# Kernel optimization log

Measured on AMD Instinct MI355X. Metric: run time of the kernel, lower is better.

## Reference

```python
import jax, jax.numpy as jnp
import numpy as np
import math

DIM = 256
N = 4096
E = 1024
NEG = -1.0e9


def setup_inputs() -> dict:
    key = jax.random.key(0)
    ks = jax.random.split(key, 10)
    x = jax.random.normal(ks[0], (N, DIM), dtype=jnp.float32)
    # sparse incidence / adjacency (module only uses >0 as mask)
    H = (jax.random.uniform(ks[1], (N, E)) < 0.05).astype(jnp.float32)
    adj = (jax.random.uniform(ks[2], (N, N)) < 0.01).astype(jnp.float32)
    s = 1.0 / math.sqrt(DIM)
    W_he = jax.random.normal(ks[3], (DIM, DIM), dtype=jnp.float32) * s  # HyperedgeAttention.W
    u = jax.random.normal(ks[4], (DIM,), dtype=jnp.float32)            # HyperedgeAttention.u
    W_e = jax.random.normal(ks[5], (DIM, DIM), dtype=jnp.float32) * s  # NodeAttention.W_e
    W_n = jax.random.normal(ks[6], (DIM, DIM), dtype=jnp.float32) * s  # NodeAttention.W_n
    W_g = jax.random.normal(ks[7], (DIM, DIM), dtype=jnp.float32) * s  # GraphAttention.W
    a_g = jax.random.normal(ks[8], (2 * DIM,), dtype=jnp.float32) * s  # GraphAttention.attn weight
    return {"x": x, "H": H, "adj": adj, "W_he": W_he, "u": u,
            "W_e": W_e, "W_n": W_n, "W_g": W_g, "a_g": a_g}


def reference(x, H, adj, W_he, u, W_e, W_n, W_g, a_g):
    n, dim = x.shape
    inv_sqrt_d = 1.0 / math.sqrt(dim)
    maskH = H > 0                       # [N,E] bool
    mask_Hf = maskH.astype(x.dtype)

    # ---- HyperedgeAttention ----
    h_he = x @ W_he                     # [N,dim]
    sc = (h_he @ u) * inv_sqrt_d        # [N]
    scE = jnp.where(maskH, sc[:, None], NEG)      # [N,E]
    A = jax.nn.softmax(scE, axis=0) * mask_Hf     # column softmax over nodes
    e_repr = A.T @ h_he                 # [E,dim]

    # ---- NodeAttention (only B is used) ----
    hn = x @ W_n                        # [N,dim]
    he = e_repr @ W_e                   # [E,dim]
    Bsc = jnp.where(maskH, (hn @ he.T) * inv_sqrt_d, NEG)
    B = jax.nn.softmax(Bsc, axis=1) * mask_Hf     # [N,E]

    # ---- GraphAttention (concat score split: e_ij = lrelu(h_i.a1 + h_j.a2)) ----
    h_g = x @ W_g                       # [N,dim]
    s1 = h_g @ a_g[:dim]                # [N]
    s2 = h_g @ a_g[dim:]                # [N]
    e = jax.nn.leaky_relu(s1[:, None] + s2[None, :], 0.2)   # [N,N]
    maskA = (adj > 0).astype(x.dtype)
    sl = jnp.eye(n, dtype=x.dtype)
    e = e * (maskA + sl) - 1e9 * jnp.clip(1.0 - maskA - sl, 0.0, None)
    G = jax.nn.softmax(e, axis=1)       # [N,N]

    # ---- Mixing ----
    he_sz = jnp.clip(mask_Hf.sum(0), 1.0, None)   # [E]
    M = (G @ mask_Hf) / he_sz[None, :]            # [N,E]
    A_hat = jax.nn.softmax(A.T + M.T, axis=1) * mask_Hf.T   # [E,N]
    e_mix = A_hat @ (x @ W_he)                    # [E,dim]
    B_hat = jax.nn.softmax(B + M, axis=1) * mask_Hf          # [N,E]
    z_h = jax.nn.elu(B_hat @ (e_mix @ W_e))       # [N,dim]
    G_hat = jax.nn.softmax(G + B @ B.T + A @ A.T, axis=1)    # [N,N]
    z_g = jax.nn.elu(G_hat @ (x @ W_g))           # [N,dim]
    return z_h, z_g
```

## Files before the change

### kernel.cpp

```cpp
#include <hip/hip_runtime.h>
#include <math.h>
#include <stdint.h>

#define Nn 4096
#define Ee 1024
#define Dd 256

typedef __attribute__((ext_vector_type(8))) __bf16 bf16x8;
typedef __attribute__((ext_vector_type(4))) float f32x4;
typedef __attribute__((ext_vector_type(8))) unsigned short u16x8;

__device__ __forceinline__ unsigned short f2bf(float f) {
  unsigned int u = __float_as_uint(f);
  unsigned int r = (u + 0x7fffu + ((u >> 16) & 1u)) >> 16;
  return (unsigned short)r;
}
__device__ __forceinline__ float bf2f(unsigned short u) {
  return __uint_as_float(((unsigned int)u) << 16);
}

__device__ __forceinline__ void gload_lds16(const void* g, void* l) {
  __builtin_amdgcn_global_load_lds(
      (__attribute__((address_space(1))) void*)const_cast<void*>(g),
      (__attribute__((address_space(3))) void*)l, 16, 0, 0);
}

__device__ __forceinline__ float block_reduce_sum(float v) {
  __shared__ float sh[4];
  #pragma unroll
  for (int o = 32; o > 0; o >>= 1) v += __shfl_down(v, o);
  int lane = threadIdx.x & 63, w = threadIdx.x >> 6;
  if (lane == 0) sh[w] = v;
  __syncthreads();
  float s = sh[0] + sh[1] + sh[2] + sh[3];
  __syncthreads();
  return s;
}

__global__ __launch_bounds__(256) void gemm_bt_bf16(
    const unsigned short* __restrict__ Ab, const unsigned short* __restrict__ Bb,
    float* __restrict__ Cp, unsigned short* __restrict__ Cb,
    int M, int N, int K, int lda, int ldb, float alpha)
{
  __shared__ unsigned short As[2][128 * 32];
  __shared__ unsigned short Bs[2][128 * 32];
  const int tid = threadIdx.x;
  const int m0 = blockIdx.x * 128, n0 = blockIdx.y * 128;
  const int wave = tid >> 6, lane = tid & 63;
  const int wr = (wave >> 1) * 64, wc = (wave & 1) * 64;
  const int l16 = lane & 15, lq = lane >> 4;
  f32x4 acc[4][4] = {};
  const int NT = K >> 5;

  auto stage = [&](int buf, int kt) {
    const int k0 = kt * 32;
    #pragma unroll
    for (int i = 0; i < 2; ++i) {
      int t2 = tid + i * 256;
      int r = t2 >> 2, c = (t2 & 3) * 8;
      gload_lds16(Ab + (size_t)(m0 + r) * lda + k0 + c, &As[buf][t2 * 8]);
    }
    #pragma unroll
    for (int i = 0; i < 2; ++i) {
      int t2 = tid + i * 256;
      int r = t2 >> 2, c = (t2 & 3) * 8;
      gload_lds16(Bb + (size_t)(n0 + r) * ldb + k0 + c, &Bs[buf][t2 * 8]);
    }
  };

  stage(0, 0);
  __syncthreads();
  int buf = 0;
  for (int kt = 0; kt < NT; ++kt) {
    if (kt + 1 < NT) stage(buf ^ 1, kt + 1);
    bf16x8 af[4], bfr[4];
    #pragma unroll
    for (int m = 0; m < 4; ++m)
      af[m] = *reinterpret_cast<const bf16x8*>(&As[buf][(wr + m * 16 + l16) * 32 + lq * 8]);
    #pragma unroll
    for (int n = 0; n < 4; ++n)
      bfr[n] = *reinterpret_cast<const bf16x8*>(&Bs[buf][(wc + n * 16 + l16) * 32 + lq * 8]);
    #pragma unroll
    for (int m = 0; m < 4; ++m)
      #pragma unroll
      for (int n = 0; n < 4; ++n)
        acc[m][n] = __builtin_amdgcn_mfma_f32_16x16x32_bf16(af[m], bfr[n], acc[m][n], 0, 0, 0);
    __syncthreads();
    buf ^= 1;
  }
  #pragma unroll
  for (int m = 0; m < 4; ++m)
    #pragma unroll
    for (int n = 0; n < 4; ++n) {
      int col = n0 + wc + n * 16 + l16;
      #pragma unroll
      for (int q = 0; q < 4; ++q) {
        int row = m0 + wr + m * 16 + lq * 4 + q;
        size_t idx = (size_t)row * N + col;
        float v = acc[m][n][q] * alpha;
        Cp[idx] = v;
        if (Cb) Cb[idx] = f2bf(v);
      }
    }
}

__global__ __launch_bounds__(256) void gemm_bts_bf16(
    const unsigned short* __restrict__ Ab, const unsigned short* __restrict__ Bb,
    float* __restrict__ Cp, int M, int N, int K, int lda, int ldb, int KS)
{
  __shared__ unsigned short As[2][128 * 32];
  __shared__ unsigned short Bs[2][128 * 32];
  const int tid = threadIdx.x;
  const int m0 = blockIdx.x * 128, n0 = blockIdx.y * 128;
  const int kbase = blockIdx.z * KS;
  const int wave = tid >> 6, lane = tid & 63;
  const int wr = (wave >> 1) * 64, wc = (wave & 1) * 64;
  const int l16 = lane & 15, lq = lane >> 4;
  f32x4 acc[4][4] = {};
  const int NT = KS >> 5;

  auto stage = [&](int buf, int kt) {
    const int k0 = kbase + kt * 32;
    #pragma unroll
    for (int i = 0; i < 2; ++i) {
      int t2 = tid + i * 256;
      int r = t2 >> 2, c = (t2 & 3) * 8;
      gload_lds16(Ab + (size_t)(m0 + r) * lda + k0 + c, &As[buf][t2 * 8]);
    }
    #pragma unroll
    for (int i = 0; i < 2; ++i) {
      int t2 = tid + i * 256;
      int r = t2 >> 2, c = (t2 & 3) * 8;
      gload_lds16(Bb + (size_t)(n0 + r) * ldb + k0 + c, &Bs[buf][t2 * 8]);
    }
  };

  stage(0, 0);
  __syncthreads();
  int buf = 0;
  for (int kt = 0; kt < NT; ++kt) {
    if (kt + 1 < NT) stage(buf ^ 1, kt + 1);
    bf16x8 af[4], bfr[4];
    #pragma unroll
    for (int m = 0; m < 4; ++m)
      af[m] = *reinterpret_cast<const bf16x8*>(&As[buf][(wr + m * 16 + l16) * 32 + lq * 8]);
    #pragma unroll
    for (int n = 0; n < 4; ++n)
      bfr[n] = *reinterpret_cast<const bf16x8*>(&Bs[buf][(wc + n * 16 + l16) * 32 + lq * 8]);
    #pragma unroll
    for (int m = 0; m < 4; ++m)
      #pragma unroll
      for (int n = 0; n < 4; ++n)
        acc[m][n] = __builtin_amdgcn_mfma_f32_16x16x32_bf16(af[m], bfr[n], acc[m][n], 0, 0, 0);
    __syncthreads();
    buf ^= 1;
  }
  #pragma unroll
  for (int m = 0; m < 4; ++m)
    #pragma unroll
    for (int n = 0; n < 4; ++n) {
      int col = n0 + wc + n * 16 + l16;
      #pragma unroll
      for (int q = 0; q < 4; ++q) {
        int row = m0 + wr + m * 16 + lq * 4 + q;
        atomicAdd(&Cp[(size_t)row * N + col], acc[m][n][q]);
      }
    }
}

__global__ __launch_bounds__(256) void gemm_gram_k(
    const unsigned short* __restrict__ CAT,
    unsigned short* __restrict__ Gb,
    float* __restrict__ rowsum)
{
  int bid = blockIdx.x;
  int by = (int)((sqrtf(8.f * bid + 1.f) - 1.f) * 0.5f);
  while ((by + 1) * (by + 2) / 2 <= bid) ++by;
  while (by * (by + 1) / 2 > bid) --by;
  int bx = bid - by * (by + 1) / 2;
  const int K = 2048;
  __shared__ unsigned short SM[17024];
  unsigned short* Asb = SM;
  unsigned short* Bsb = SM + 8192;
  const int tid = threadIdx.x;
  const int m0 = bx * 128, n0 = by * 128;
  const int wave = tid >> 6, lane = tid & 63;
  const int wr = (wave >> 1) * 64, wc = (wave & 1) * 64;
  const int l16 = lane & 15, lq = lane >> 4;
  f32x4 acc[4][4] = {};
  const int NT = K >> 5;

  auto stage = [&](int buf, int kt) {
    const int k0 = kt * 32;
    #pragma unroll
    for (int i = 0; i < 2; ++i) {
      int t2 = tid + i * 256;
      int r = t2 >> 2, c = (t2 & 3) * 8;
      gload_lds16(CAT + (size_t)(m0 + r) * K + k0 + c, Asb + buf * 4096 + t2 * 8);
    }
    #pragma unroll
    for (int i = 0; i < 2; ++i) {
      int t2 = tid + i * 256;
      int r = t2 >> 2, c = (t2 & 3) * 8;
      gload_lds16(CAT + (size_t)(n0 + r) * K + k0 + c, Bsb + buf * 4096 + t2 * 8);
    }
  };

  stage(0, 0);
  __syncthreads();
  int buf = 0;
  for (int kt = 0; kt < NT; ++kt) {
    if (kt + 1 < NT) stage(buf ^ 1, kt + 1);
    bf16x8 af[4], bfr[4];
    #pragma unroll
    for (int m = 0; m < 4; ++m)
      af[m] = *reinterpret_cast<const bf16x8*>(Asb + buf * 4096 + (wr + m * 16 + l16) * 32 + lq * 8);
    #pragma unroll
    for (int n = 0; n < 4; ++n)
      bfr[n] = *reinterpret_cast<const bf16x8*>(Bsb + buf * 4096 + (wc + n * 16 + l16) * 32 + lq * 8);
    #pragma unroll
    for (int m = 0; m < 4; ++m)
      #pragma unroll
      for (int n = 0; n < 4; ++n)
        acc[m][n] = __builtin_amdgcn_mfma_f32_16x16x32_bf16(af[m], bfr[n], acc[m][n], 0, 0, 0);
    __syncthreads();
    buf ^= 1;
  }
  #pragma unroll
  for (int m = 0; m < 4; ++m)
    #pragma unroll
    for (int q = 0; q < 4; ++q) {
      int row = m0 + wr + m * 16 + lq * 4 + q;
      float s = 0.f;
      #pragma unroll
      for (int n = 0; n < 4; ++n) {
        int col = n0 + wc + n * 16 + l16;
        size_t idx = (size_t)row * Nn + col;
        float e = expf(bf2f(Gb[idx]) + acc[m][n][q]);
        Gb[idx] = f2bf(e);
        s += e;
      }
      s += __shfl_xor(s, 1); s += __shfl_xor(s, 2);
      s += __shfl_xor(s, 4); s += __shfl_xor(s, 8);
      if (l16 == 0) atomicAdd(&rowsum[row], s);
    }
  if (bx == by) return;

  __syncthreads();
  unsigned short* Tg = SM;
  {
    int cc = tid >> 1, r0 = (tid & 1) * 64;
    const unsigned short* src = Gb + (size_t)(n0 + cc) * Nn + m0 + r0;
    unsigned short* dst = Tg + cc * 132 + r0;
    #pragma unroll
    for (int v = 0; v < 8; ++v)
      *reinterpret_cast<u16x8*>(dst + v * 8) = *reinterpret_cast<const u16x8*>(src + v * 8);
  }
  __syncthreads();
  #pragma unroll
  for (int n = 0; n < 4; ++n) {
    int ccl = wc + n * 16 + l16;
    float cs = 0.f;
    #pragma unroll
    for (int m = 0; m < 4; ++m) {
      int sa = ccl * 132 + wr + m * 16 + lq * 4;
      ushort4 lg = *reinterpret_cast<const ushort4*>(&Tg[sa]);
      ushort4 eo;
      float e0 = expf(bf2f(lg.x) + acc[m][n][0]); eo.x = f2bf(e0); cs += e0;
      float e1 = expf(bf2f(lg.y) + acc[m][n][1]); eo.y = f2bf(e1); cs += e1;
      float e2 = expf(bf2f(lg.z) + acc[m][n][2]); eo.z = f2bf(e2); cs += e2;
      float e3 = expf(bf2f(lg.w) + acc[m][n][3]); eo.w = f2bf(e3); cs += e3;
      *reinterpret_cast<ushort4*>(&Tg[sa]) = eo;
    }
    cs += __shfl_xor(cs, 16); cs += __shfl_xor(cs, 32);
    if (lq == 0) atomicAdd(&rowsum[n0 + ccl], cs);
  }
  __syncthreads();
  {
    int cc = tid >> 1, r0 = (tid & 1) * 64;
    const unsigned short* src = Tg + cc * 132 + r0;
    unsigned short* dst = Gb + (size_t)(n0 + cc) * Nn + m0 + r0;
    #pragma unroll
    for (int v = 0; v < 8; ++v)
      *reinterpret_cast<u16x8*>(dst + v * 8) = *reinterpret_cast<const u16x8*>(src + v * 8);
  }
}

__global__ __launch_bounds__(256) void gemm64s_bt_bf16(
    const unsigned short* __restrict__ Ab, const unsigned short* __restrict__ Bb,
    float* __restrict__ Cp, int M, int N, int K, int KS)
{
  __shared__ unsigned short As[2][64 * 64];
  __shared__ unsigned short Bs[2][64 * 64];
  const int tid = threadIdx.x;
  const int m0 = blockIdx.x * 64, n0 = blockIdx.y * 64;
  const int kbase = blockIdx.z * KS;
  const int wave = tid >> 6, lane = tid & 63;
  const int wr = (wave >> 1) * 32, wc = (wave & 1) * 32;
  const int l16 = lane & 15, lq = lane >> 4;
  f32x4 acc[2][2] = {};
  const int NT = KS >> 6;

  auto stage = [&](int buf, int kt) {
    const int k0 = kbase + kt * 64;
    #pragma unroll
    for (int i = 0; i < 2; ++i) {
      int t2 = tid + i * 256;
      int r = t2 >> 3, c = (t2 & 7) * 8;
      gload_lds16(Ab + (size_t)(m0 + r) * K + k0 + c, &As[buf][t2 * 8]);
    }
    #pragma unroll
    for (int i = 0; i < 2; ++i) {
      int t2 = tid + i * 256;
      int r = t2 >> 3, c = (t2 & 7) * 8;
      gload_lds16(Bb + (size_t)(n0 + r) * K + k0 + c, &Bs[buf][t2 * 8]);
    }
  };

  stage(0, 0);
  __syncthreads();
  int buf = 0;
  for (int kt = 0; kt < NT; ++kt) {
    if (kt + 1 < NT) stage(buf ^ 1, kt + 1);
    bf16x8 af[2][2], bfr[2][2];
    #pragma unroll
    for (int m = 0; m < 2; ++m)
      #pragma unroll
      for (int ks = 0; ks < 2; ++ks)
        af[m][ks] = *reinterpret_cast<const bf16x8*>(
            &As[buf][(wr + m * 16 + l16) * 64 + ks * 32 + lq * 8]);
    #pragma unroll
    for (int n = 0; n < 2; ++n)
      #pragma unroll
      for (int ks = 0; ks < 2; ++ks)
        bfr[n][ks] = *reinterpret_cast<const bf16x8*>(
            &Bs[buf][(wc + n * 16 + l16) * 64 + ks * 32 + lq * 8]);
    #pragma unroll
    for (int m = 0; m < 2; ++m)
      #pragma unroll
      for (int n = 0; n < 2; ++n)
        #pragma unroll
        for (int ks = 0; ks < 2; ++ks)
          acc[m][n] = __builtin_amdgcn_mfma_f32_16x16x32_bf16(af[m][ks], bfr[n][ks], acc[m][n], 0, 0, 0);
    __syncthreads();
    buf ^= 1;
  }
  #pragma unroll
  for (int m = 0; m < 2; ++m)
    #pragma unroll
    for (int n = 0; n < 2; ++n) {
      int col = n0 + wc + n * 16 + l16;
      #pragma unroll
      for (int q = 0; q < 4; ++q) {
        int row = m0 + wr + m * 16 + lq * 4 + q;
        atomicAdd(&Cp[(size_t)row * N + col], acc[m][n][q]);
      }
    }
}

__global__ __launch_bounds__(256) void cvt_bf16_k(const float* __restrict__ in,
                                                  unsigned short* __restrict__ out, long n) {
  long i = ((long)blockIdx.x * 256 + threadIdx.x) * 8;
  if (i + 8 > n) return;
  float4 a = *reinterpret_cast<const float4*>(&in[i]);
  float4 b = *reinterpret_cast<const float4*>(&in[i + 4]);
  u16x8 o;
  o[0] = f2bf(a.x); o[1] = f2bf(a.y); o[2] = f2bf(a.z); o[3] = f2bf(a.w);
  o[4] = f2bf(b.x); o[5] = f2bf(b.y); o[6] = f2bf(b.z); o[7] = f2bf(b.w);
  *reinterpret_cast<u16x8*>(&out[i]) = o;
}

__global__ __launch_bounds__(256) void tcvt_k(const float* __restrict__ in,
                                              unsigned short* __restrict__ outT, int R, int S,
                                              const float* __restrict__ coldiv) {
  __shared__ unsigned short tile[64][65];
  int r0 = blockIdx.x * 64, c0 = blockIdx.y * 64;
  int t = threadIdx.x & 63, q = threadIdx.x >> 6;
  float sc = coldiv ? 1.f / fmaxf(coldiv[c0 + t], 1.f) : 1.f;
  for (int rr = q; rr < 64; rr += 4)
    tile[t][rr] = f2bf(in[(long)(r0 + rr) * S + c0 + t] * sc);
  __syncthreads();
  for (int cc = q; cc < 64; cc += 4)
    outT[(long)(c0 + cc) * R + r0 + t] = tile[cc][t];
}

__global__ __launch_bounds__(256) void elu_rows_k(float* __restrict__ p,
                                                  const float* __restrict__ rowsum) {
  long i = ((long)blockIdx.x * 256 + threadIdx.x) * 4;
  float4 v = *reinterpret_cast<const float4*>(&p[i]);
  float sc = 1.f;
  long half = (long)Nn * Dd;
  if (i >= half) sc = 1.f / rowsum[(i - half) >> 8];
  v.x *= sc; v.y *= sc; v.z *= sc; v.w *= sc;
  v.x = v.x > 0.f ? v.x : expm1f(v.x);
  v.y = v.y > 0.f ? v.y : expm1f(v.y);
  v.z = v.z > 0.f ? v.z : expm1f(v.z);
  v.w = v.w > 0.f ? v.w : expm1f(v.w);
  *reinterpret_cast<float4*>(&p[i]) = v;
}

__global__ __launch_bounds__(256) void gemm64_k(
    const float* __restrict__ Ap, const float* __restrict__ Bp, float* __restrict__ Cp,
    int M, int N, int K, int Asm, int Ask, int Bsk, int Bsn)
{
  __shared__ alignas(16) float As[16][68];
  __shared__ alignas(16) float Bs[16][68];
  const int tid = threadIdx.x;
  const int tx = tid & 15, ty = tid >> 4;
  const int m0 = blockIdx.x * 64, n0 = blockIdx.y * 64;
  float acc[4][4] = {};
  for (int k0 = 0; k0 < K; k0 += 16) {
    if (Ask == 1) {
      int mm = tid >> 2, kk = (tid & 3) << 2;
      float4 v = *reinterpret_cast<const float4*>(&Ap[(long)(m0 + mm) * Asm + k0 + kk]);
      As[kk + 0][mm] = v.x; As[kk + 1][mm] = v.y; As[kk + 2][mm] = v.z; As[kk + 3][mm] = v.w;
    } else {
      int kk = tid >> 4, mm = (tid & 15) << 2;
      *reinterpret_cast<float4*>(&As[kk][mm]) =
          *reinterpret_cast<const float4*>(&Ap[(long)(k0 + kk) * Ask + m0 + mm]);
    }
    if (Bsn == 1) {
      int kk = tid >> 4, nn = (tid & 15) << 2;
      *reinterpret_cast<float4*>(&Bs[kk][nn]) =
          *reinterpret_cast<const float4*>(&Bp[(long)(k0 + kk) * Bsk + n0 + nn]);
    } else {
      int nn = tid >> 2, kk = (tid & 3) << 2;
      float4 v = *reinterpret_cast<const float4*>(&Bp[(long)(n0 + nn) * Bsn + k0 + kk]);
      Bs[kk + 0][nn] = v.x; Bs[kk + 1][nn] = v.y; Bs[kk + 2][nn] = v.z; Bs[kk + 3][nn] = v.w;
    }
    __syncthreads();
    #pragma unroll
    for (int kk = 0; kk < 16; ++kk) {
      float4 av = *reinterpret_cast<const float4*>(&As[kk][ty << 2]);
      float4 bv = *reinterpret_cast<const float4*>(&Bs[kk][tx << 2]);
      float a[4] = {av.x, av.y, av.z, av.w};
      float b[4] = {bv.x, bv.y, bv.z, bv.w};
      #pragma unroll
      for (int r = 0; r < 4; ++r)
        #pragma unroll
        for (int c = 0; c < 4; ++c) acc[r][c] = fmaf(a[r], b[c], acc[r][c]);
    }
    __syncthreads();
  }
  #pragma unroll
  for (int r = 0; r < 4; ++r) {
    long base = (long)(m0 + (ty << 2) + r) * N + n0 + (tx << 2);
    float4 o = {acc[r][0], acc[r][1], acc[r][2], acc[r][3]};
    *reinterpret_cast<float4*>(&Cp[base]) = o;
  }
}

__global__ __launch_bounds__(256) void rowdots_k(
    const float* __restrict__ hcat, const float* __restrict__ u, const float* __restrict__ a_g,
    float* __restrict__ esc, float* __restrict__ s1, float* __restrict__ s2)
{
  int i = blockIdx.x, t = threadIdx.x;
  float hh = hcat[(long)i * 1024 + t];
  float hg = hcat[(long)i * 1024 + 512 + t];
  float d0 = block_reduce_sum(hh * u[t]);
  float d1 = block_reduce_sum(hg * a_g[t]);
  float d2 = block_reduce_sum(hg * a_g[Dd + t]);
  if (t == 0) {
    esc[i] = expf(d0 * 0.0625f);
    s1[i] = d1;
    s2[i] = d2;
  }
}

__global__ __launch_bounds__(256) void colstats_k(
    const float* __restrict__ H, const float* __restrict__ esc,
    float* __restrict__ colden, float* __restrict__ cnt)
{
  int e = blockIdx.x * 256 + threadIdx.x;
  int r0 = blockIdx.y * 128;
  float d = 0.f, c = 0.f;
  for (int r = r0; r < r0 + 128; ++r) {
    float h = H[(long)r * Ee + e];
    if (h > 0.f) { d += esc[r]; c += 1.f; }
  }
  atomicAdd(&colden[e], d);
  atomicAdd(&cnt[e], c);
}

__global__ __launch_bounds__(256) void fillA_k(
    const float* __restrict__ H, const float* __restrict__ esc,
    const float* __restrict__ colden,
    unsigned short* __restrict__ CAT, unsigned short* __restrict__ AbT)
{
  __shared__ unsigned short tile[64][68];
  int r0 = blockIdx.x * 64, e0 = blockIdx.y * 64;
  int te = threadIdx.x & 63, tq = threadIdx.x >> 6;
  float cd = colden[e0 + te];
  for (int rr = tq; rr < 64; rr += 4) {
    long idx = (long)(r0 + rr) * Ee + e0 + te;
    float h = H[idx];
    float val = h > 0.f ? esc[r0 + rr] / cd : 0.f;
    unsigned short vb = f2bf(val);
    CAT[(long)(r0 + rr) * 2048 + 1024 + e0 + te] = vb;
    tile[te][rr] = vb;
  }
  __syncthreads();
  for (int ee = tq; ee < 64; ee += 4)
    AbT[(long)(e0 + ee) * Nn + r0 + te] = tile[ee][te];
}

__global__ __launch_bounds__(256) void brow_k(const float* __restrict__ Bbuf,
                                              const float* __restrict__ H,
                                              unsigned short* __restrict__ CAT)
{
  int i = blockIdx.x, t = threadIdx.x;
  long base = (long)i * Ee + t * 4;
  float4 raw = *reinterpret_cast<const float4*>(&Bbuf[base]);
  float4 h = *reinterpret_cast<const float4*>(&H[base]);
  float rr[4] = {raw.x, raw.y, raw.z, raw.w}, hh[4] = {h.x, h.y, h.z, h.w};
  float p[4]; float s = 0.f;
  #pragma unroll
  for (int k = 0; k < 4; ++k) { p[k] = hh[k] > 0.f ? expf(rr[k]) : 0.f; s += p[k]; }
  float den = block_reduce_sum(s);
  float inv = den > 0.f ? 1.f / den : 0.f;
  ushort4 ob = {f2bf(p[0] * inv), f2bf(p[1] * inv), f2bf(p[2] * inv), f2bf(p[3] * inv)};
  *reinterpret_cast<ushort4*>(&CAT[(long)i * 2048 + t * 4]) = ob;
}

__global__ __launch_bounds__(256) void gfill_k(
    const float* __restrict__ adj, const float* __restrict__ s1,
    const float* __restrict__ s2, unsigned short* __restrict__ Gb)
{
  int i = blockIdx.x, t = threadIdx.x;
  float s1i = s1[i];
  float p[16]; float sum = 0.f;
  #pragma unroll
  for (int c = 0; c < 4; ++c) {
    int j = c * 1024 + t * 4;
    float4 a = *reinterpret_cast<const float4*>(&adj[(long)i * Nn + j]);
    float4 sv = *reinterpret_cast<const float4*>(&s2[j]);
    float aa[4] = {a.x, a.y, a.z, a.w}, ss[4] = {sv.x, sv.y, sv.z, sv.w};
    #pragma unroll
    for (int k = 0; k < 4; ++k) {
      float f = (aa[k] > 0.f ? 1.f : 0.f) + ((j + k) == i ? 1.f : 0.f);
      float l = s1i + ss[k];
      l = l > 0.f ? l : 0.2f * l;
      float val = l * f - 1e9f * fmaxf(1.f - f, 0.f);
      float pp = expf(val);
      p[c * 4 + k] = pp; sum += pp;
    }
  }
  float den = block_reduce_sum(sum);
  float inv = 1.f / den;
  #pragma unroll
  for (int c = 0; c < 4; ++c) {
    int j = c * 1024 + t * 4;
    ushort4 ob = {f2bf(p[c * 4] * inv), f2bf(p[c * 4 + 1] * inv),
                  f2bf(p[c * 4 + 2] * inv), f2bf(p[c * 4 + 3] * inv)};
    *reinterpret_cast<ushort4*>(&Gb[(long)i * Nn + j]) = ob;
  }
}

__global__ __launch_bounds__(256) void amstats_k(
    const unsigned short* __restrict__ CAT, const float* __restrict__ Mm,
    float* __restrict__ aden)
{
  int e = blockIdx.x * 256 + threadIdx.x;
  int r0 = blockIdx.y * 128;
  float d = 0.f;
  for (int r = r0; r < r0 + 128; ++r)
    d += expf(bf2f(CAT[(size_t)r * 2048 + 1024 + e]) + Mm[(size_t)r * Ee + e]);
  atomicAdd(&aden[e], d);
}

__global__ __launch_bounds__(256) void ahat_k(
    const unsigned short* __restrict__ CAT, const float* __restrict__ Mm,
    const float* __restrict__ H, const float* __restrict__ aden,
    unsigned short* __restrict__ AhB)
{
  __shared__ float tile[64][65];
  int j0 = blockIdx.x * 64, e0 = blockIdx.y * 64;
  int te = threadIdx.x & 63;
  int tq = threadIdx.x >> 6;
  int e = e0 + te;
  float inv = 1.f / aden[e];
  for (int jj = tq; jj < 64; jj += 4) {
    long idx = (long)(j0 + jj) * Ee + e;
    float a = bf2f(CAT[(size_t)(j0 + jj) * 2048 + 1024 + e]);
    float val = (H[idx] > 0.f) ? expf(a + Mm[idx]) * inv : 0.f;
    tile[te][jj] = val;
  }
  __syncthreads();
  for (int ee = tq; ee < 64; ee += 4)
    AhB[(long)(e0 + ee) * Nn + j0 + te] = f2bf(tile[ee][te]);
}

__global__ __launch_bounds__(256) void bhat_k(const unsigned short* __restrict__ CAT,
                                              const float* __restrict__ Mm,
                                              const float* __restrict__ H,
                                              unsigned short* __restrict__ Bb2)
{
  int i = blockIdx.x, t = threadIdx.x;
  long base = (long)i * Ee + t * 4;
  ushort4 bu = *reinterpret_cast<const ushort4*>(&CAT[(long)i * 2048 + t * 4]);
  float4 m = *reinterpret_cast<const float4*>(&Mm[base]);
  float4 h = *reinterpret_cast<const float4*>(&H[base]);
  float bb[4] = {bf2f(bu.x), bf2f(bu.y), bf2f(bu.z), bf2f(bu.w)};
  float mm2[4] = {m.x, m.y, m.z, m.w}, hh[4] = {h.x, h.y, h.z, h.w};
  float p[4]; float s = 0.f;
  #pragma unroll
  for (int k = 0; k < 4; ++k) { p[k] = expf(bb[k] + mm2[k]); s += p[k]; }
  float den = block_reduce_sum(s);
  float inv = 1.f / den;
  #pragma unroll
  for (int k = 0; k < 4; ++k) p[k] = hh[k] > 0.f ? p[k] * inv : 0.f;
  ushort4 ob = {f2bf(p[0]), f2bf(p[1]), f2bf(p[2]), f2bf(p[3])};
  *reinterpret_cast<ushort4*>(&Bb2[base]) = ob;
}

extern "C" void kernel_launch(void* const* d_in, const int* in_sizes, int n_in,
                              void* d_out, int out_size, void* d_ws, size_t ws_size,
                              hipStream_t stream) {
  const float* x    = (const float*)d_in[0];
  const float* H    = (const float*)d_in[1];
  const float* adj  = (const float*)d_in[2];
  const float* W_he = (const float*)d_in[3];
  const float* u    = (const float*)d_in[4];
  const float* W_e  = (const float*)d_in[5];
  const float* W_n  = (const float*)d_in[6];
  const float* W_g  = (const float*)d_in[7];
  const float* a_g  = (const float*)d_in[8];
  float* out = (float*)d_out;
  float* ws  = (float*)d_ws;
  (void)in_sizes; (void)n_in; (void)out_size; (void)ws_size;

  size_t off = 0;
  auto alloc = [&](size_t n) { float* p = ws + off; off += n; return p; };
  float* hcat4  = alloc((size_t)Nn * 1024);
  float* Wp     = alloc((size_t)Dd * Dd);
  float* esc    = alloc(Nn);
  float* s1     = alloc(Nn);
  float* s2     = alloc(Nn);
  float* colden = alloc(Ee);
  float* cnt    = alloc(Ee);
  float* aden   = alloc(Ee);
  float* rowsum = alloc(Nn);
  float* heb    = alloc((size_t)Ee * Dd);
  float* tewTf  = alloc((size_t)Dd * Ee);
  float* Bbuf   = alloc((size_t)Nn * Ee);
  float* Mm     = alloc((size_t)Nn * Ee);
  unsigned short* Gb    = (unsigned short*)alloc((size_t)Nn * Nn / 2);
  unsigned short* CAT   = (unsigned short*)alloc((size_t)Nn * 2048 / 2);
  unsigned short* Hbt   = (unsigned short*)alloc((size_t)Ee * Nn / 2);
  unsigned short* AbT   = (unsigned short*)alloc((size_t)Ee * Nn / 2);
  unsigned short* AhB   = (unsigned short*)alloc((size_t)Ee * Nn / 2);
  unsigned short* hWT   = (unsigned short*)alloc((size_t)Dd * Nn / 2);
  unsigned short* hgT   = (unsigned short*)alloc((size_t)Dd * Nn / 2);
  unsigned short* tewT  = (unsigned short*)alloc((size_t)Dd * Ee / 2);
  unsigned short* Bb2   = (unsigned short*)alloc((size_t)Nn * Ee / 2);
  unsigned short* xb    = (unsigned short*)alloc((size_t)Nn * Dd / 2);
  unsigned short* WcTb4 = (unsigned short*)alloc((size_t)1024 * Dd / 2);
  unsigned short* hcatB = (unsigned short*)alloc((size_t)Nn * 1024 / 2);
  unsigned short* hebB  = (unsigned short*)alloc((size_t)Ee * Dd / 2);

  hipMemsetAsync(colden, 0, (3 * Ee + Nn) * sizeof(float), stream);
  hipMemsetAsync(heb, 0, 2 * (size_t)Ee * Dd * sizeof(float), stream);
  hipMemsetAsync(Mm, 0, (size_t)Nn * Ee * sizeof(float), stream);
  hipMemsetAsync(out, 0, 2 * (size_t)Nn * Dd * sizeof(float), stream);

  auto gbt = [&](const unsigned short* A, const unsigned short* B, float* C, unsigned short* Cb,
                 int M, int N, int K, int lda, int ldb, float alpha) {
    gemm_bt_bf16<<<dim3(M / 128, N / 128), 256, 0, stream>>>(A, B, C, Cb, M, N, K, lda, ldb, alpha);
  };
  auto gs64 = [&](const unsigned short* A, const unsigned short* B, float* C,
                  int M, int N, int K, int KS) {
    gemm64s_bt_bf16<<<dim3(M / 64, N / 64, K / KS), 256, 0, stream>>>(A, B, C, M, N, K, KS);
  };
  auto tcvt = [&](const float* in, unsigned short* o, int R, int S, int cols, const float* cd) {
    tcvt_k<<<dim3(R / 64, cols / 64), 256, 0, stream>>>(in, o, R, S, cd);
  };

  gemm64_k<<<dim3(4, 4), 256, 0, stream>>>(W_he, W_e, Wp, Dd, Dd, Dd, Dd, 1, Dd, 1);
  cvt_bf16_k<<<(Nn * Dd) / 2048, 256, 0, stream>>>(x, xb, (long)Nn * Dd);
  tcvt(W_he, WcTb4, Dd, Dd, Dd, nullptr);
  tcvt(W_n, WcTb4 + 1 * 256 * 256, Dd, Dd, Dd, nullptr);
  tcvt(W_g, WcTb4 + 2 * 256 * 256, Dd, Dd, Dd, nullptr);
  tcvt(Wp, WcTb4 + 3 * 256 * 256, Dd, Dd, Dd, nullptr);
  gbt(xb, WcTb4, hcat4, hcatB, Nn, 1024, Dd, Dd, Dd, 1.f);
  rowdots_k<<<Nn, 256, 0, stream>>>(hcat4, u, a_g, esc, s1, s2);
  colstats_k<<<dim3(Ee / 256, 32), 256, 0, stream>>>(H, esc, colden, cnt);
  fillA_k<<<dim3(Nn / 64, Ee / 64), 256, 0, stream>>>(H, esc, colden, CAT, AbT);
  tcvt(hcat4 + 768, hWT, Nn, 1024, Dd, nullptr);
  gs64(AbT, hWT, heb, Ee, Dd, Nn, 512);
  cvt_bf16_k<<<(Ee * Dd) / 2048, 256, 0, stream>>>(heb, hebB, (long)Ee * Dd);
  gbt(hcatB + 256, hebB, Bbuf, nullptr, Nn, Ee, Dd, 1024, Dd, 0.0625f);
  brow_k<<<Nn, 256, 0, stream>>>(Bbuf, H, CAT);
  gfill_k<<<Nn, 256, 0, stream>>>(adj, s1, s2, Gb);
  tcvt(H, Hbt, Nn, Ee, Ee, cnt);
  gemm_bts_bf16<<<dim3(Nn / 128, Ee / 128, 2), 256, 0, stream>>>(Gb, Hbt, Mm, Nn, Ee, Nn, Nn, Nn, 2048);
  gemm_gram_k<<<528, 256, 0, stream>>>(CAT, Gb, rowsum);
  amstats_k<<<dim3(Ee / 256, 32), 256, 0, stream>>>(CAT, Mm, aden);
  ahat_k<<<dim3(Nn / 64, Ee / 64), 256, 0, stream>>>(CAT, Mm, H, aden, AhB);
  gs64(hWT, AhB, tewTf, Dd, Ee, Nn, 512);
  cvt_bf16_k<<<(Dd * Ee) / 2048, 256, 0, stream>>>(tewTf, tewT, (long)Dd * Ee);
  bhat_k<<<Nn, 256, 0, stream>>>(CAT, Mm, H, Bb2);
  gs64(Bb2, tewT, out, Nn, Dd, Ee, 512);
  tcvt(hcat4 + 512, hgT, Nn, 1024, Dd, nullptr);
  gs64(Gb, hgT, out + (size_t)Nn * Dd, Nn, Dd, Nn, 1024);
  elu_rows_k<<<(2 * Nn * Dd) / 1024, 256, 0, stream>>>(out, rowsum);
}
```

Measured before the change: 587.3 us.

## Batch transpose-convert launches, remap gram block order, use 128-tile split-K GEMM

Four separate weight transpose-convert launches become one batched kernel, and the two hcat4 transposes become another batched kernel placed earlier. The triangular gram kernel's block index is permuted with a stride-66 interleave, likely so neighbouring blocks spread across XCDs or improve cache locality. The final G_hat@h_g GEMM moves from the 64-tile split-K kernel to the 128-tile split-K kernel with K split 512. The aim is fewer launches and better tile efficiency, at the cost of more atomic partial-sum traffic on the output.

Measured after the change: 586.6 us. No clear change (-0.1%).

```diff
diff --git a/kernel.cpp b/kernel.cpp
--- a/kernel.cpp
+++ b/kernel.cpp
@@ -173,7 +173,7 @@
     unsigned short* __restrict__ Gb,
     float* __restrict__ rowsum)
 {
-  int bid = blockIdx.x;
+  int bid = (blockIdx.x & 7) * 66 + (blockIdx.x >> 3);
   int by = (int)((sqrtf(8.f * bid + 1.f) - 1.f) * 0.5f);
   while ((by + 1) * (by + 2) / 2 <= bid) ++by;
   while (by * (by + 1) / 2 > bid) --by;
@@ -382,6 +382,40 @@
   __syncthreads();
   for (int cc = q; cc < 64; cc += 4)
     outT[(long)(c0 + cc) * R + r0 + t] = tile[cc][t];
+}
+
+__global__ __launch_bounds__(256) void tcvtW_k(const float* __restrict__ W0,
+                                               const float* __restrict__ W1,
+                                               const float* __restrict__ W2,
+                                               const float* __restrict__ W3,
+                                               unsigned short* __restrict__ outT) {
+  __shared__ unsigned short tile[64][65];
+  int s = blockIdx.z;
+  const float* in = s == 0 ? W0 : (s == 1 ? W1 : (s == 2 ? W2 : W3));
+  unsigned short* o = outT + (size_t)s * 256 * 256;
+  int r0 = blockIdx.x * 64, c0 = blockIdx.y * 64;
+  int t = threadIdx.x & 63, q = threadIdx.x >> 6;
+  for (int rr = q; rr < 64; rr += 4)
+    tile[t][rr] = f2bf(in[(long)(r0 + rr) * Dd + c0 + t]);
+  __syncthreads();
+  for (int cc = q; cc < 64; cc += 4)
+    o[(long)(c0 + cc) * Dd + r0 + t] = tile[cc][t];
+}
+
+__global__ __launch_bounds__(256) void tcvtH_k(const float* __restrict__ hcat4,
+                                               unsigned short* __restrict__ hWT,
+                                               unsigned short* __restrict__ hgT) {
+  __shared__ unsigned short tile[64][65];
+  int s = blockIdx.z;
+  const float* in = hcat4 + (s == 0 ? 768 : 512);
+  unsigned short* o = s == 0 ? hWT : hgT;
+  int r0 = blockIdx.x * 64, c0 = blockIdx.y * 64;
+  int t = threadIdx.x & 63, q = threadIdx.x >> 6;
+  for (int rr = q; rr < 64; rr += 4)
+    tile[t][rr] = f2bf(in[(long)(r0 + rr) * 1024 + c0 + t]);
+  __syncthreads();
+  for (int cc = q; cc < 64; cc += 4)
+    o[(long)(c0 + cc) * Nn + r0 + t] = tile[cc][t];
 }
 
 __global__ __launch_bounds__(256) void elu_rows_k(float* __restrict__ p,
@@ -667,6 +701,10 @@
                  int M, int N, int K, int lda, int ldb, float alpha) {
     gemm_bt_bf16<<<dim3(M / 128, N / 128), 256, 0, stream>>>(A, B, C, Cb, M, N, K, lda, ldb, alpha);
   };
+  auto gbts = [&](const unsigned short* A, const unsigned short* B, float* C,
+                  int M, int N, int K, int lda, int ldb, int KS) {
+    gemm_bts_bf16<<<dim3(M / 128, N / 128, K / KS), 256, 0, stream>>>(A, B, C, M, N, K, lda, ldb, KS);
+  };
   auto gs64 = [&](const unsigned short* A, const unsigned short* B, float* C,
                   int M, int N, int K, int KS) {
     gemm64s_bt_bf16<<<dim3(M / 64, N / 64, K / KS), 256, 0, stream>>>(A, B, C, M, N, K, KS);
@@ -677,22 +715,19 @@
 
   gemm64_k<<<dim3(4, 4), 256, 0, stream>>>(W_he, W_e, Wp, Dd, Dd, Dd, Dd, 1, Dd, 1);
   cvt_bf16_k<<<(Nn * Dd) / 2048, 256, 0, stream>>>(x, xb, (long)Nn * Dd);
-  tcvt(W_he, WcTb4, Dd, Dd, Dd, nullptr);
-  tcvt(W_n, WcTb4 + 1 * 256 * 256, Dd, Dd, Dd, nullptr);
-  tcvt(W_g, WcTb4 + 2 * 256 * 256, Dd, Dd, Dd, nullptr);
-  tcvt(Wp, WcTb4 + 3 * 256 * 256, Dd, Dd, Dd, nullptr);
+  tcvtW_k<<<dim3(4, 4, 4), 256, 0, stream>>>(W_he, W_n, W_g, Wp, WcTb4);
   gbt(xb, WcTb4, hcat4, hcatB, Nn, 1024, Dd, Dd, Dd, 1.f);
   rowdots_k<<<Nn, 256, 0, stream>>>(hcat4, u, a_g, esc, s1, s2);
+  tcvtH_k<<<dim3(Nn / 64, Dd / 64, 2), 256, 0, stream>>>(hcat4, hWT, hgT);
   colstats_k<<<dim3(Ee / 256, 32), 256, 0, stream>>>(H, esc, colden, cnt);
   fillA_k<<<dim3(Nn / 64, Ee / 64), 256, 0, stream>>>(H, esc, colden, CAT, AbT);
-  tcvt(hcat4 + 768, hWT, Nn, 1024, Dd, nullptr);
   gs64(AbT, hWT, heb, Ee, Dd, Nn, 512);
   cvt_bf16_k<<<(Ee * Dd) / 2048, 256, 0, stream>>>(heb, hebB, (long)Ee * Dd);
   gbt(hcatB + 256, hebB, Bbuf, nullptr, Nn, Ee, Dd, 1024, Dd, 0.0625f);
   brow_k<<<Nn, 256, 0, stream>>>(Bbuf, H, CAT);
   gfill_k<<<Nn, 256, 0, stream>>>(adj, s1, s2, Gb);
   tcvt(H, Hbt, Nn, Ee, Ee, cnt);
-  gemm_bts_bf16<<<dim3(Nn / 128, Ee / 128, 2), 256, 0, stream>>>(Gb, Hbt, Mm, Nn, Ee, Nn, Nn, Nn, 2048);
+  gbts(Gb, Hbt, Mm, Nn, Ee, Nn, Nn, Nn, 2048);
   gemm_gram_k<<<528, 256, 0, stream>>>(CAT, Gb, rowsum);
   amstats_k<<<dim3(Ee / 256, 32), 256, 0, stream>>>(CAT, Mm, aden);
   ahat_k<<<dim3(Nn / 64, Ee / 64), 256, 0, stream>>>(CAT, Mm, H, aden, AhB);
@@ -700,7 +735,6 @@
   cvt_bf16_k<<<(Dd * Ee) / 2048, 256, 0, stream>>>(tewTf, tewT, (long)Dd * Ee);
   bhat_k<<<Nn, 256, 0, stream>>>(CAT, Mm, H, Bb2);
   gs64(Bb2, tewT, out, Nn, Dd, Ee, 512);
-  tcvt(hcat4 + 512, hgT, Nn, 1024, Dd, nullptr);
-  gs64(Gb, hgT, out + (size_t)Nn * Dd, Nn, Dd, Nn, 1024);
+  gbts(Gb, hgT, out + (size_t)Nn * Dd, Nn, Dd, Nn, Nn, Nn, 512);
   elu_rows_k<<<(2 * Nn * Dd) / 1024, 256, 0, stream>>>(out, rowsum);
 }
```
